# Performance work log

Hardware: AMD Instinct MI355X
Metric: run time of the kernel (lower is better)

The kernel has to match this reference:

```python
import jax, jax.numpy as jnp
import numpy as np

N0, N1, N2 = 120000, 30000, 6000   # node frontier sizes per hop
E0, E1 = 480000, 96000             # sampled edges per layer (~fanout 16)
D = 128                            # in_channels == hidden_size
R = 8                              # num_relations
NB = 4                             # num_bases
ETOT = 3000000                     # global edge count (edge_type_all)


def setup_inputs() -> dict:
    key = jax.random.key(0)
    ks = jax.random.split(key, 24)
    s = 1.0 / np.sqrt(D)
    f32 = jnp.float32
    inp = {
        "x": jax.random.normal(ks[0], (N0, D), dtype=f32),
        "src0": jax.random.randint(ks[1], (E0,), 0, N0),
        "dst0": jax.random.randint(ks[2], (E0,), 0, N1),
        "e_id0": jax.random.randint(ks[3], (E0,), 0, ETOT),
        "src1": jax.random.randint(ks[4], (E1,), 0, N1),
        "dst1": jax.random.randint(ks[5], (E1,), 0, N2),
        "e_id1": jax.random.randint(ks[6], (E1,), 0, ETOT),
        "edge_type_all": jax.random.randint(ks[7], (ETOT,), 0, R),
        # pre_layer: linear + relu
        "pre_W": jax.random.normal(ks[8], (D, D), dtype=f32) * s,
        "pre_b": jnp.zeros((D,), f32),
        # RGCNConv layer 0 (basis decomposition)
        "basis0": jax.random.normal(ks[9], (NB, D, D), dtype=f32) * s,
        "comp0": jax.random.normal(ks[10], (R, NB), dtype=f32) * (1.0 / np.sqrt(NB)),
        "root0": jax.random.normal(ks[11], (D, D), dtype=f32) * s,
        "bias0": jnp.zeros((D,), f32),
        "g0": jnp.ones((D,), f32),
        "be0": jnp.zeros((D,), f32),
        # RGCNConv layer 1
        "basis1": jax.random.normal(ks[12], (NB, D, D), dtype=f32) * s,
        "comp1": jax.random.normal(ks[13], (R, NB), dtype=f32) * (1.0 / np.sqrt(NB)),
        "root1": jax.random.normal(ks[14], (D, D), dtype=f32) * s,
        "bias1": jnp.zeros((D,), f32),
        "g1": jnp.ones((D,), f32),
        "be1": jnp.zeros((D,), f32),
        # post_layer: single linear
        "post_W": jax.random.normal(ks[15], (D, D), dtype=f32) * s,
        "post_b": jnp.zeros((D,), f32),
    }
    return inp


def _layernorm(x, g, b, eps=1e-5):
    mu = jnp.mean(x, axis=-1, keepdims=True)
    var = jnp.mean(jnp.square(x - mu), axis=-1, keepdims=True)
    return (x - mu) * jax.lax.rsqrt(var + eps) * g + b


def _rgcn_conv(x, n_dst, src, dst, etype, basis, comp, root, bias):
    # Bipartite RGCNConv with basis decomposition and mean aggregation.
    # Since messages W[r] @ x[src] are linear, aggregate per relation first
    # (segment_sum of raw features), then apply the relation weight once.
    x_t = x[:n_dst]                                    # [n_dst, D]
    out = x_t @ root + bias                            # root/self transform
    W = jnp.einsum('rb,bio->rio', comp, basis)         # [R, D, D]
    x_j = x[src]                                       # [E, D] gather
    deg = jax.ops.segment_sum(jnp.ones(src.shape[0], x.dtype), dst,
                              num_segments=n_dst)      # mean over all relations
    agg = jnp.zeros((n_dst, W.shape[-1]), x.dtype)
    for r in range(W.shape[0]):                        # R=8 structurally distinct
        m = (etype == r).astype(x.dtype)[:, None]
        s_r = jax.ops.segment_sum(x_j * m, dst, num_segments=n_dst)
        agg = agg + s_r @ W[r]
    return out + agg / jnp.maximum(deg, 1.0)[:, None]


def reference(x, src0, dst0, e_id0, src1, dst1, e_id1, edge_type_all,
              pre_W, pre_b, basis0, comp0, root0, bias0, g0, be0,
              basis1, comp1, root1, bias1, g1, be1, post_W, post_b):
    # pre_layer: linear + relu (GeneralMultiLayer, final_act=True)
    h = jax.nn.relu(x @ pre_W + pre_b)
    # layer 0: edge-type gather -> relational conv -> norm -> act (eval: no dropout)
    h = _rgcn_conv(h, N1, src0, dst0, edge_type_all[e_id0],
                   basis0, comp0, root0, bias0)
    h = jax.nn.relu(_layernorm(h, g0, be0))
    # layer 1
    h = _rgcn_conv(h, N2, src1, dst1, edge_type_all[e_id1],
                   basis1, comp1, root1, bias1)
    h = jax.nn.relu(_layernorm(h, g1, be1))
    # post_layer: single linear MLP
    return h @ post_W + post_b
```

## Files before the change

### kernel.cpp

```cpp
#include <hip/hip_runtime.h>
#include <cstdint>

#define DD 128
#define CAP 64
#define E0C 480000
#define E1C 96000
#define N0C 120000
#define N1C 30000
#define N2C 6000

typedef unsigned short u16;
typedef __attribute__((ext_vector_type(8))) short bf16x8;
typedef __attribute__((ext_vector_type(16))) float f32x16;

__device__ __forceinline__ u16 f2b(float f) {
    union { float f; unsigned u; } a; a.f = f;
    unsigned r = (a.u + 0x7fffu + ((a.u >> 16) & 1u)) >> 16;
    return (u16)r;
}
__device__ __forceinline__ float b2f(u16 u) {
    union { unsigned u; float f; } a; a.u = ((unsigned)u) << 16;
    return a.f;
}

struct WtJob { const float* src[12]; };
__global__ __launch_bounds__(256) void prep_kernel(
    WtJob job, u16* __restrict__ dst, int* __restrict__ cnt0, int* __restrict__ cnt1)
{
    int gtid = blockIdx.x * 256 + threadIdx.x;
    for (int i = gtid; i < N1C + N2C; i += 256 * 256) {
        if (i < N1C) cnt0[i] = 0; else cnt1[i - N1C] = 0;
    }
    if (blockIdx.x >= 192) return;
    __shared__ float tile[32][33];
    int m = blockIdx.x >> 4;
    int t4 = blockIdx.x & 15;
    int tr = (t4 >> 2) * 32;
    int tc = (t4 & 3) * 32;
    int lx = threadIdx.x & 31, ly = threadIdx.x >> 5;
    #pragma unroll
    for (int yy = 0; yy < 32; yy += 8)
        tile[ly + yy][lx] = job.src[m][(tr + ly + yy) * DD + tc + lx];
    __syncthreads();
    int tid = threadIdx.x;
    if (tid < 128) {
        int nl = tid >> 2, kch = tid & 3;
        int k = tr + kch * 8, n = tc + nl;
        int kc = k >> 4, half = (k >> 3) & 1;
        int t = n >> 5, l31 = n & 31;
        bf16x8 pk;
        #pragma unroll
        for (int j = 0; j < 8; ++j) pk[j] = (short)f2b(tile[kch * 8 + j][nl]);
        *(bf16x8*)(dst + (size_t)m * 16384 + kc * 2048 + t * 512 + half * 256 + l31 * 8) = pk;
    }
}

__global__ __launch_bounds__(64) void pre_fill_kernel(
    const float* __restrict__ x,
    const int* __restrict__ src0, const int* __restrict__ dst0, const int* __restrict__ eid0,
    const int* __restrict__ src1, const int* __restrict__ dst1, const int* __restrict__ eid1,
    const int* __restrict__ etype,
    int* __restrict__ cnt0, int* __restrict__ cnt1,
    int* __restrict__ ep0, int* __restrict__ ep1,
    const u16* __restrict__ Wr, const float* __restrict__ bias,
    u16* __restrict__ h0)
{
    int gtid = blockIdx.x * 64 + threadIdx.x;
    int nthr = gridDim.x * 64;
    for (int e = gtid; e < E0C + E1C; e += nthr) {
        bool L0 = e < E0C;
        int ee = L0 ? e : e - E0C;
        int d   = L0 ? dst0[ee] : dst1[ee];
        int eid = L0 ? eid0[ee] : eid1[ee];
        int s   = L0 ? src0[ee] : src1[ee];
        int r = etype[eid];
        int* cnt = L0 ? cnt0 : cnt1;
        int* ep  = L0 ? ep0  : ep1;
        int pos = atomicAdd(&cnt[d], 1);
        if (pos < CAP) ep[(size_t)d * CAP + pos] = s | (r << 28);
    }

    int lane = threadIdx.x & 63;
    int l31 = lane & 31, half = lane >> 5;
    int m0 = blockIdx.x * 32;
    if (m0 >= N0C) return;
    int arow = m0 + l31;
    bool rv = arow < N0C;
    f32x16 acc[4];
    #pragma unroll
    for (int t = 0; t < 4; ++t)
        #pragma unroll
        for (int i = 0; i < 16; ++i) acc[t][i] = 0.f;

    const float* Aq = x + (size_t)arow * DD;
    float4 st[16];
    if (rv) {
        #pragma unroll
        for (int c = 0; c < 16; ++c)
            st[c] = *(const float4*)(Aq + ((c >> 1) * 16 + half * 8) + (c & 1) * 4);
    } else {
        #pragma unroll
        for (int c = 0; c < 16; ++c) st[c] = make_float4(0.f, 0.f, 0.f, 0.f);
    }
    #pragma unroll
    for (int kc = 0; kc < 8; ++kc) {
        bf16x8 bfr[4];
        #pragma unroll
        for (int t = 0; t < 4; ++t)
            bfr[t] = *(const bf16x8*)(Wr + (size_t)((kc * 4 + t) * 64 + lane) * 8);
        float4 u0 = st[2 * kc], u1 = st[2 * kc + 1];
        bf16x8 af;
        af[0] = (short)f2b(u0.x); af[1] = (short)f2b(u0.y);
        af[2] = (short)f2b(u0.z); af[3] = (short)f2b(u0.w);
        af[4] = (short)f2b(u1.x); af[5] = (short)f2b(u1.y);
        af[6] = (short)f2b(u1.z); af[7] = (short)f2b(u1.w);
        #pragma unroll
        for (int t = 0; t < 4; ++t)
            acc[t] = __builtin_amdgcn_mfma_f32_32x32x16_bf16(af, bfr[t], acc[t], 0, 0, 0);
    }

    float bb[4];
    #pragma unroll
    for (int t = 0; t < 4; ++t) bb[t] = bias[t * 32 + l31];
    #pragma unroll
    for (int reg = 0; reg < 16; ++reg) {
        int rl = (reg & 3) + 8 * (reg >> 2) + 4 * half;
        int row = m0 + rl;
        if (row < N0C) {
            #pragma unroll
            for (int t = 0; t < 4; ++t)
                h0[(size_t)row * DD + t * 32 + l31] =
                    f2b(fmaxf(acc[t][reg] + bb[t], 0.f));
        }
    }
}

__global__ __launch_bounds__(256) void agg_kernel(
    const u16* __restrict__ h, const int* __restrict__ cnt,
    const int* __restrict__ ep, const float* __restrict__ comp,
    u16* __restrict__ T, int ndst)
{
    __shared__ float4 cmp4[8];
    if (threadIdx.x < 8) cmp4[threadIdx.x] = ((const float4*)comp)[threadIdx.x];
    __syncthreads();
    int row = blockIdx.x * 4 + (threadIdx.x >> 6);
    if (row >= ndst) return;
    int lane = threadIdx.x & 63;
    int n = cnt[row];
    int end = n < CAP ? n : CAP;
    const int* erow = ep + (size_t)row * CAP;
    float a0[4] = {0.f, 0.f, 0.f, 0.f};
    float a1[4] = {0.f, 0.f, 0.f, 0.f};
    int j = 0;
    for (; j + 16 <= end; j += 16) {
        int vv[16]; unsigned gg[16];
        #pragma unroll
        for (int u = 0; u < 16; ++u) vv[u] = erow[j + u];
        #pragma unroll
        for (int u = 0; u < 16; ++u)
            gg[u] = *(const unsigned*)(h + (size_t)(vv[u] & 0x0FFFFFFF) * DD + 2 * lane);
        #pragma unroll
        for (int u = 0; u < 16; ++u) {
            float4 c = cmp4[vv[u] >> 28];
            float x0 = b2f((u16)(gg[u] & 0xffffu));
            float x1 = b2f((u16)(gg[u] >> 16));
            a0[0] = fmaf(c.x, x0, a0[0]); a1[0] = fmaf(c.x, x1, a1[0]);
            a0[1] = fmaf(c.y, x0, a0[1]); a1[1] = fmaf(c.y, x1, a1[1]);
            a0[2] = fmaf(c.z, x0, a0[2]); a1[2] = fmaf(c.z, x1, a1[2]);
            a0[3] = fmaf(c.w, x0, a0[3]); a1[3] = fmaf(c.w, x1, a1[3]);
        }
    }
    for (; j + 4 <= end; j += 4) {
        int vv[4]; unsigned gg[4];
        #pragma unroll
        for (int u = 0; u < 4; ++u) vv[u] = erow[j + u];
        #pragma unroll
        for (int u = 0; u < 4; ++u)
            gg[u] = *(const unsigned*)(h + (size_t)(vv[u] & 0x0FFFFFFF) * DD + 2 * lane);
        #pragma unroll
        for (int u = 0; u < 4; ++u) {
            float4 c = cmp4[vv[u] >> 28];
            float x0 = b2f((u16)(gg[u] & 0xffffu));
            float x1 = b2f((u16)(gg[u] >> 16));
            a0[0] = fmaf(c.x, x0, a0[0]); a1[0] = fmaf(c.x, x1, a1[0]);
            a0[1] = fmaf(c.y, x0, a0[1]); a1[1] = fmaf(c.y, x1, a1[1]);
            a0[2] = fmaf(c.z, x0, a0[2]); a1[2] = fmaf(c.z, x1, a1[2]);
            a0[3] = fmaf(c.w, x0, a0[3]); a1[3] = fmaf(c.w, x1, a1[3]);
        }
    }
    for (; j < end; ++j) {
        int v = erow[j];
        unsigned g = *(const unsigned*)(h + (size_t)(v & 0x0FFFFFFF) * DD + 2 * lane);
        float4 c = cmp4[v >> 28];
        float x0 = b2f((u16)(g & 0xffffu));
        float x1 = b2f((u16)(g >> 16));
        a0[0] = fmaf(c.x, x0, a0[0]); a1[0] = fmaf(c.x, x1, a1[0]);
        a0[1] = fmaf(c.y, x0, a0[1]); a1[1] = fmaf(c.y, x1, a1[1]);
        a0[2] = fmaf(c.z, x0, a0[2]); a1[2] = fmaf(c.z, x1, a1[2]);
        a0[3] = fmaf(c.w, x0, a0[3]); a1[3] = fmaf(c.w, x1, a1[3]);
    }
    float inv = 1.f / fmaxf((float)n, 1.f);
    #pragma unroll
    for (int b = 0; b < 4; ++b) {
        unsigned pk = (unsigned)f2b(a0[b] * inv) | ((unsigned)f2b(a1[b] * inv) << 16);
        *(unsigned*)(T + ((size_t)b * ndst + row) * DD + 2 * lane) = pk;
    }
}

template<bool OBF16, bool LN>
__global__ __launch_bounds__(64) void mfma_gemm(
    const u16* __restrict__ Ap, int nplanes, const u16* __restrict__ Ar,
    const u16* __restrict__ Wp, const u16* __restrict__ Wr,
    const float* __restrict__ bias, const float* __restrict__ gw,
    const float* __restrict__ bw, void* __restrict__ Cv, int nrows)
{
    int lane = threadIdx.x & 63;
    int l31 = lane & 31, half = lane >> 5;
    int m0 = blockIdx.x * 32;
    int arow = m0 + l31;
    bool rv = arow < nrows;
    f32x16 acc[4];
    #pragma unroll
    for (int t = 0; t < 4; ++t)
        #pragma unroll
        for (int i = 0; i < 16; ++i) acc[t][i] = 0.f;

    bf16x8 A0[8], A1[8];
    {
        const u16* Ainit = (nplanes == 0) ? Ar : Ap;
        if (rv) {
            #pragma unroll
            for (int c = 0; c < 8; ++c)
                A0[c] = *(const bf16x8*)(Ainit + (size_t)arow * DD + c * 16 + half * 8);
        } else {
            #pragma unroll
            for (int c = 0; c < 8; ++c) A0[c] = (bf16x8){0,0,0,0,0,0,0,0};
        }
    }
    for (int p = 0; p <= nplanes; ++p) {
        const u16* Wsel = (p == nplanes) ? Wr : Wp + p * 16384;
        if (p < nplanes) {
            const u16* An = (p + 1 == nplanes) ? Ar : Ap + (size_t)(p + 1) * nrows * DD;
            if (rv) {
                #pragma unroll
                for (int c = 0; c < 8; ++c)
                    A1[c] = *(const bf16x8*)(An + (size_t)arow * DD + c * 16 + half * 8);
            } else {
                #pragma unroll
                for (int c = 0; c < 8; ++c) A1[c] = (bf16x8){0,0,0,0,0,0,0,0};
            }
        }
        #pragma unroll
        for (int kc = 0; kc < 8; ++kc) {
            bf16x8 bfr[4];
            #pragma unroll
            for (int t = 0; t < 4; ++t)
                bfr[t] = *(const bf16x8*)(Wsel + (size_t)((kc * 4 + t) * 64 + lane) * 8);
            #pragma unroll
            for (int t = 0; t < 4; ++t)
                acc[t] = __builtin_amdgcn_mfma_f32_32x32x16_bf16(A0[kc], bfr[t], acc[t], 0, 0, 0);
        }
        if (p < nplanes) {
            #pragma unroll
            for (int c = 0; c < 8; ++c) A0[c] = A1[c];
        }
    }

    float bb[4];
    #pragma unroll
    for (int t = 0; t < 4; ++t) bb[t] = bias[t * 32 + l31];
    float gg[4], ww[4];
    if (LN) {
        #pragma unroll
        for (int t = 0; t < 4; ++t) { gg[t] = gw[t * 32 + l31]; ww[t] = bw[t * 32 + l31]; }
    }

    #pragma unroll
    for (int reg = 0; reg < 16; ++reg) {
        int rl = (reg & 3) + 8 * (reg >> 2) + 4 * half;
        int row = m0 + rl;
        float v[4];
        #pragma unroll
        for (int t = 0; t < 4; ++t) v[t] = acc[t][reg] + bb[t];
        if (LN) {
            float s1 = 0.f, s2 = 0.f;
            #pragma unroll
            for (int t = 0; t < 4; ++t) { s1 += v[t]; s2 += v[t] * v[t]; }
            #pragma unroll
            for (int o = 1; o < 32; o <<= 1) {
                s1 += __shfl_xor(s1, o);
                s2 += __shfl_xor(s2, o);
            }
            float mu = s1 * (1.f / 128.f);
            float var = s2 * (1.f / 128.f) - mu * mu;
            float rstd = rsqrtf(fmaxf(var, 0.f) + 1e-5f);
            #pragma unroll
            for (int t = 0; t < 4; ++t)
                v[t] = fmaxf((v[t] - mu) * rstd * gg[t] + ww[t], 0.f);
        }
        if (row < nrows) {
            #pragma unroll
            for (int t = 0; t < 4; ++t) {
                if (OBF16) ((u16*)Cv)[(size_t)row * DD + t * 32 + l31] = f2b(v[t]);
                else       ((float*)Cv)[(size_t)row * DD + t * 32 + l31] = v[t];
            }
        }
    }
}

extern "C" void kernel_launch(void* const* d_in, const int* in_sizes, int n_in,
                              void* d_out, int out_size, void* d_ws, size_t ws_size,
                              hipStream_t stream)
{
    const float* x     = (const float*)d_in[0];
    const int* src0    = (const int*)d_in[1];
    const int* dst0    = (const int*)d_in[2];
    const int* eid0    = (const int*)d_in[3];
    const int* src1    = (const int*)d_in[4];
    const int* dst1    = (const int*)d_in[5];
    const int* eid1    = (const int*)d_in[6];
    const int* etype   = (const int*)d_in[7];
    const float* preW  = (const float*)d_in[8];
    const float* preb  = (const float*)d_in[9];
    const float* basis0 = (const float*)d_in[10];
    const float* comp0  = (const float*)d_in[11];
    const float* root0  = (const float*)d_in[12];
    const float* bias0  = (const float*)d_in[13];
    const float* g0    = (const float*)d_in[14];
    const float* be0   = (const float*)d_in[15];
    const float* basis1 = (const float*)d_in[16];
    const float* comp1  = (const float*)d_in[17];
    const float* root1  = (const float*)d_in[18];
    const float* bias1  = (const float*)d_in[19];
    const float* g1    = (const float*)d_in[20];
    const float* be1   = (const float*)d_in[21];
    const float* postW = (const float*)d_in[22];
    const float* postb = (const float*)d_in[23];
    float* out = (float*)d_out;

    char* ws = (char*)d_ws;
    size_t o = 0;
    auto alloc = [&](size_t bytes) { char* p = ws + o; o += (bytes + 255) & ~(size_t)255; return p; };
    u16* h0   = (u16*)alloc((size_t)N0C * DD * 2);
    u16* T0   = (u16*)alloc((size_t)4 * N1C * DD * 2);
    u16* h1   = (u16*)alloc((size_t)N1C * DD * 2);
    u16* T1   = (u16*)alloc((size_t)4 * N2C * DD * 2);
    u16* h2   = (u16*)alloc((size_t)N2C * DD * 2);
    u16* wt   = (u16*)alloc((size_t)12 * 16384 * 2);
    int* cnt0 = (int*)alloc((size_t)N1C * 4);
    int* cnt1 = (int*)alloc((size_t)N2C * 4);
    int* ep0  = (int*)alloc((size_t)N1C * CAP * 4);
    int* ep1  = (int*)alloc((size_t)N2C * CAP * 4);

    WtJob job;
    job.src[0] = preW;
    for (int b = 0; b < 4; ++b) job.src[1 + b] = basis0 + (size_t)b * 16384;
    job.src[5] = root0;
    for (int b = 0; b < 4; ++b) job.src[6 + b] = basis1 + (size_t)b * 16384;
    job.src[10] = root1;
    job.src[11] = postW;

    prep_kernel<<<256, 256, 0, stream>>>(job, wt, cnt0, cnt1);
    pre_fill_kernel<<<(N0C + 31) / 32, 64, 0, stream>>>(
        x, src0, dst0, eid0, src1, dst1, eid1, etype,
        cnt0, cnt1, ep0, ep1, wt + 0 * 16384, preb, h0);
    agg_kernel<<<(N1C + 3) / 4, 256, 0, stream>>>(h0, cnt0, ep0, comp0, T0, N1C);
    mfma_gemm<true, true><<<(N1C + 31) / 32, 64, 0, stream>>>(
        T0, 4, h0, wt + 1 * 16384, wt + 5 * 16384, bias0, g0, be0, h1, N1C);
    agg_kernel<<<(N2C + 3) / 4, 256, 0, stream>>>(h1, cnt1, ep1, comp1, T1, N2C);
    mfma_gemm<true, true><<<(N2C + 31) / 32, 64, 0, stream>>>(
        T1, 4, h1, wt + 6 * 16384, wt + 10 * 16384, bias1, g1, be1, h2, N2C);
    mfma_gemm<false, false><<<(N2C + 31) / 32, 64, 0, stream>>>(
        nullptr, 0, h2, nullptr, wt + 11 * 16384, postb, nullptr, nullptr, out, N2C);
}
```

Before: 308.0 us.

## Split edge bucketing and pre-layer GEMM into separate block roles

The fused pre_fill kernel used to make every 64-thread block do a grid-stride share of the edge bucketing and then its GEMM tile. Now the first 128 blocks of 256 threads only bucket edges, with the loop unrolled 4x so loads, etype gathers and atomics can overlap. The remaining blocks run four GEMM waves each. This separates the latency-bound atomic work from the MFMA work and batches memory requests, but concentrates the edge work on fewer blocks, which could leave it as a tail.

Result: faster. 294.8 us (-4.3%).

```diff
diff --git a/kernel.cpp b/kernel.cpp
--- a/kernel.cpp
+++ b/kernel.cpp
@@ -3,6 +3,7 @@
 
 #define DD 128
 #define CAP 64
+#define ESB 128
 #define E0C 480000
 #define E1C 96000
 #define N0C 120000
@@ -55,7 +56,7 @@
     }
 }
 
-__global__ __launch_bounds__(64) void pre_fill_kernel(
+__global__ __launch_bounds__(256) void pre_fill_kernel(
     const float* __restrict__ x,
     const int* __restrict__ src0, const int* __restrict__ dst0, const int* __restrict__ eid0,
     const int* __restrict__ src1, const int* __restrict__ dst1, const int* __restrict__ eid1,
@@ -65,32 +66,56 @@
     const u16* __restrict__ Wr, const float* __restrict__ bias,
     u16* __restrict__ h0)
 {
-    int gtid = blockIdx.x * 64 + threadIdx.x;
-    int nthr = gridDim.x * 64;
-    for (int e = gtid; e < E0C + E1C; e += nthr) {
-        bool L0 = e < E0C;
-        int ee = L0 ? e : e - E0C;
-        int d   = L0 ? dst0[ee] : dst1[ee];
-        int eid = L0 ? eid0[ee] : eid1[ee];
-        int s   = L0 ? src0[ee] : src1[ee];
-        int r = etype[eid];
-        int* cnt = L0 ? cnt0 : cnt1;
-        int* ep  = L0 ? ep0  : ep1;
-        int pos = atomicAdd(&cnt[d], 1);
-        if (pos < CAP) ep[(size_t)d * CAP + pos] = s | (r << 28);
-    }
-
+    if (blockIdx.x < ESB) {
+        const int STR = ESB * 256;
+        int gtid = blockIdx.x * 256 + threadIdx.x;
+        int e = gtid;
+        for (; e + 3 * STR < E0C + E1C; e += 4 * STR) {
+            int d[4], eidv[4], s[4], r[4], pos[4];
+            bool L0[4];
+            #pragma unroll
+            for (int u = 0; u < 4; ++u) {
+                int idx = e + u * STR;
+                L0[u] = idx < E0C;
+                int ee = L0[u] ? idx : idx - E0C;
+                d[u]    = L0[u] ? dst0[ee] : dst1[ee];
+                eidv[u] = L0[u] ? eid0[ee] : eid1[ee];
+                s[u]    = L0[u] ? src0[ee] : src1[ee];
+            }
+            #pragma unroll
+            for (int u = 0; u < 4; ++u) r[u] = etype[eidv[u]];
+            #pragma unroll
+            for (int u = 0; u < 4; ++u)
+                pos[u] = atomicAdd(L0[u] ? &cnt0[d[u]] : &cnt1[d[u]], 1);
+            #pragma unroll
+            for (int u = 0; u < 4; ++u) {
+                if (pos[u] < CAP) {
+                    int* ep = L0[u] ? ep0 : ep1;
+                    ep[(size_t)d[u] * CAP + pos[u]] = s[u] | (r[u] << 28);
+                }
+            }
+        }
+        for (; e < E0C + E1C; e += STR) {
+            bool L0 = e < E0C;
+            int ee = L0 ? e : e - E0C;
+            int d   = L0 ? dst0[ee] : dst1[ee];
+            int eid = L0 ? eid0[ee] : eid1[ee];
+            int s   = L0 ? src0[ee] : src1[ee];
+            int r = etype[eid];
+            int pos = atomicAdd(L0 ? &cnt0[d] : &cnt1[d], 1);
+            if (pos < CAP) (L0 ? ep0 : ep1)[(size_t)d * CAP + pos] = s | (r << 28);
+        }
+        return;
+    }
+
+    int bid = blockIdx.x - ESB;
+    int wave = threadIdx.x >> 6;
     int lane = threadIdx.x & 63;
     int l31 = lane & 31, half = lane >> 5;
-    int m0 = blockIdx.x * 32;
+    int m0 = (bid * 4 + wave) * 32;
     if (m0 >= N0C) return;
     int arow = m0 + l31;
     bool rv = arow < N0C;
-    f32x16 acc[4];
-    #pragma unroll
-    for (int t = 0; t < 4; ++t)
-        #pragma unroll
-        for (int i = 0; i < 16; ++i) acc[t][i] = 0.f;
 
     const float* Aq = x + (size_t)arow * DD;
     float4 st[16];
@@ -102,6 +127,11 @@
         #pragma unroll
         for (int c = 0; c < 16; ++c) st[c] = make_float4(0.f, 0.f, 0.f, 0.f);
     }
+    f32x16 accs[4];
+    #pragma unroll
+    for (int t = 0; t < 4; ++t)
+        #pragma unroll
+        for (int i = 0; i < 16; ++i) accs[t][i] = 0.f;
     #pragma unroll
     for (int kc = 0; kc < 8; ++kc) {
         bf16x8 bfr[4];
@@ -116,9 +146,8 @@
         af[6] = (short)f2b(u1.z); af[7] = (short)f2b(u1.w);
         #pragma unroll
         for (int t = 0; t < 4; ++t)
-            acc[t] = __builtin_amdgcn_mfma_f32_32x32x16_bf16(af, bfr[t], acc[t], 0, 0, 0);
-    }
-
+            accs[t] = __builtin_amdgcn_mfma_f32_32x32x16_bf16(af, bfr[t], accs[t], 0, 0, 0);
+    }
     float bb[4];
     #pragma unroll
     for (int t = 0; t < 4; ++t) bb[t] = bias[t * 32 + l31];
@@ -130,7 +159,7 @@
             #pragma unroll
             for (int t = 0; t < 4; ++t)
                 h0[(size_t)row * DD + t * 32 + l31] =
-                    f2b(fmaxf(acc[t][reg] + bb[t], 0.f));
+                    f2b(fmaxf(accs[t][reg] + bb[t], 0.f));
         }
     }
 }
@@ -361,7 +390,7 @@
     job.src[11] = postW;
 
     prep_kernel<<<256, 256, 0, stream>>>(job, wt, cnt0, cnt1);
-    pre_fill_kernel<<<(N0C + 31) / 32, 64, 0, stream>>>(
+    pre_fill_kernel<<<ESB + (N0C + 127) / 128, 256, 0, stream>>>(
         x, src0, dst0, eid0, src1, dst1, eid1, etype,
         cnt0, cnt1, ep0, ep1, wt + 0 * 16384, preb, h0);
     agg_kernel<<<(N1C + 3) / 4, 256, 0, stream>>>(h0, cnt0, ep0, comp0, T0, N1C);
```
